# Performance work log

Hardware: AMD Instinct MI355X
Metric: run time of the kernel (lower is better)

## Reference

```python
import jax, jax.numpy as jnp
import numpy as np

B, T, D, HD, O = 32, 2000, 80, 512, 512
H = HD // 2  # per-direction hidden


def setup_inputs() -> dict:
    key = jax.random.key(0)
    ks = jax.random.split(key, 20)
    x = jax.random.normal(ks[0], (B, T, D), jnp.float32)
    x_len = jax.random.randint(ks[1], (B,), T // 2, T + 1)
    s = 1.0 / np.sqrt(H)
    def u(k, shape):
        return jax.random.uniform(k, shape, jnp.float32, -s, s)
    return {
        'x': x, 'x_len': x_len,
        # BLSTM1 (input D), fwd/bwd directions; b is (b_ih + b_hh) combined
        'Wih1f': u(ks[2], (4 * H, D)), 'Whh1f': u(ks[3], (4 * H, H)), 'b1f': u(ks[4], (4 * H,)),
        'Wih1b': u(ks[5], (4 * H, D)), 'Whh1b': u(ks[6], (4 * H, H)), 'b1b': u(ks[7], (4 * H,)),
        # BLSTM2 (input HD)
        'Wih2f': u(ks[8], (4 * H, HD)), 'Whh2f': u(ks[9], (4 * H, H)), 'b2f': u(ks[10], (4 * H,)),
        'Wih2b': u(ks[11], (4 * H, HD)), 'Whh2b': u(ks[12], (4 * H, H)), 'b2b': u(ks[13], (4 * H,)),
        'Wlin': u(ks[14], (O, HD)), 'blin': u(ks[15], (O,)),
    }


def _lstm(x, mask, Wih, Whh, b):
    # x: [B,T,D], mask: [B,T] bool. Packed semantics: state frozen and output 0 at padded steps.
    Bs = x.shape[0]
    Hs = Whh.shape[1]
    xg = jnp.einsum('btd,gd->btg', x, Wih) + b  # precompute input projection [B,T,4H]
    def step(carry, inp):
        h, c = carry
        xt, mt = inp
        g = xt + h @ Whh.T
        i, f, gg, o = jnp.split(g, 4, axis=-1)  # PyTorch gate order i,f,g,o
        c_n = jax.nn.sigmoid(f) * c + jax.nn.sigmoid(i) * jnp.tanh(gg)
        h_n = jax.nn.sigmoid(o) * jnp.tanh(c_n)
        m = mt[:, None]
        h = jnp.where(m, h_n, h)
        c = jnp.where(m, c_n, c)
        return (h, c), h * m
    h0 = jnp.zeros((Bs, Hs), x.dtype)
    _, ys = jax.lax.scan(step, (h0, h0), (xg.transpose(1, 0, 2), mask.T))
    return ys.transpose(1, 0, 2)


def _rev(x, lengths):
    # per-sequence time reversal of the valid prefix
    Ts = x.shape[1]
    t = jnp.arange(Ts)
    idx = jnp.clip(lengths[:, None] - 1 - t[None, :], 0, Ts - 1)
    return jnp.take_along_axis(x, idx[..., None], axis=1)


def _blstm(x, lengths, Wf, Uf, bf, Wb, Ub, bb):
    Ts = x.shape[1]
    mask = jnp.arange(Ts)[None, :] < lengths[:, None]
    fwd = _lstm(x, mask, Wf, Uf, bf)
    bwd = _rev(_lstm(_rev(x, lengths), mask, Wb, Ub, bb), lengths) * mask[..., None]
    return jnp.concatenate([fwd, bwd], axis=-1)


def _pool(x, s):
    # MaxPool1d(kernel=s, stride=s, pad=0) over time of [B,T,C]
    if s == 1:
        return x
    Bs, Ts, Cs = x.shape
    To = Ts // s
    return x[:, :To * s].reshape(Bs, To, s, Cs).max(axis=2)


def reference(x, x_len, Wih1f, Whh1f, b1f, Wih1b, Whh1b, b1b,
              Wih2f, Whh2f, b2f, Wih2b, Whh2b, b2b, Wlin, blin):
    s1, s2 = 2, 1  # closest_factors(time_reduction=2)
    out = _blstm(x, x_len, Wih1f, Whh1f, b1f, Wih1b, Whh1b, b1b)
    out = _pool(out, s1)
    lens = x_len // s1  # (L - k)//s + 1 == L//s when k==s, pad=0, dil=1
    out = _blstm(out, lens, Wih2f, Whh2f, b2f, Wih2b, Whh2b, b2b)
    out = _pool(out, s2)
    lens = lens // s2
    out = out @ Wlin.T + blin  # dropout is identity in eval mode
    return out, lens
```

## Files before the change

### kernel.cpp

```cpp
#include <hip/hip_runtime.h>


typedef _Float16 h2_t __attribute__((ext_vector_type(2)));

constexpr int RC = 10;
constexpr int AC = 15;
constexpr int LC = 7;

__device__ __forceinline__ float dot2acc(unsigned int w, unsigned int h, float acc) {
  h2_t wv = __builtin_bit_cast(h2_t, w);
  h2_t hv = __builtin_bit_cast(h2_t, h);
#if __has_builtin(__builtin_amdgcn_fdot2)
  return __builtin_amdgcn_fdot2(wv, hv, acc, false);
#else
  return acc + (float)wv[0] * (float)hv[0] + (float)wv[1] * (float)hv[1];
#endif
}

__device__ __forceinline__ float dot8(uint4 w, uint4 h, float acc) {
  acc = dot2acc(w.x, h.x, acc);
  acc = dot2acc(w.y, h.y, acc);
  acc = dot2acc(w.z, h.z, acc);
  acc = dot2acc(w.w, h.w, acc);
  return acc;
}

__device__ __forceinline__ float sigf(float x) { return 1.f / (1.f + __expf(-x)); }

__global__ __launch_bounds__(256) void pack_w(const float* __restrict__ W,
                                              uint4* __restrict__ Wp, int K) {
  const int idx = blockIdx.x * 256 + threadIdx.x;
  const int total = (K >> 3) << 10;
  if (idx >= total) return;
  const int g = idx & 1023;
  const int k8 = idx >> 10;
  const float* src = W + (size_t)g * K + k8 * 8;
  h2_t p0, p1, p2, p3;
  p0[0] = (_Float16)src[0]; p0[1] = (_Float16)src[1];
  p1[0] = (_Float16)src[2]; p1[1] = (_Float16)src[3];
  p2[0] = (_Float16)src[4]; p2[1] = (_Float16)src[5];
  p3[0] = (_Float16)src[6]; p3[1] = (_Float16)src[7];
  uint4 o;
  o.x = __builtin_bit_cast(unsigned int, p0);
  o.y = __builtin_bit_cast(unsigned int, p1);
  o.z = __builtin_bit_cast(unsigned int, p2);
  o.w = __builtin_bit_cast(unsigned int, p3);
  Wp[(size_t)k8 * 1024 + g] = o;
}

__global__ __launch_bounds__(256) void pack_flat(const float* __restrict__ src,
                                                 _Float16* __restrict__ dst, int n) {
  const int i = blockIdx.x * 256 + threadIdx.x;
  if (i < n) dst[i] = (_Float16)src[i];
}

__global__ __launch_bounds__(256) void zero16(uint4* __restrict__ p, int n16) {
  const int i = blockIdx.x * 256 + threadIdx.x;
  if (i < n16) { uint4 z; z.x = z.y = z.z = z.w = 0u; p[i] = z; }
}

template <typename AT, typename CT>
__global__ __launch_bounds__(256) void gemm_any(
    const AT* __restrict__ A, const float* __restrict__ B,
    const float* __restrict__ bias, CT* __restrict__ C,
    int M, int N, int K, int Twin, int Tfull, int t0, int REV,
    const int* __restrict__ x_len, int lensh) {
  __shared__ float As[16][128];
  __shared__ float Bs[16][64];
  const int tid = threadIdx.x;
  const int m0 = blockIdx.y * 128, n0 = blockIdx.x * 64;
  const int ra = tid >> 1;
  const int ca = (tid & 1) * 8;
  const int rb = tid >> 2;
  const int cb = (tid & 3) * 4;
  const int ty = tid >> 4;
  const int tx = tid & 15;
  const int am = m0 + ra;
  int arow = am;
  if (Twin > 0) {
    const int bb = am / Twin;
    int ti = t0 + (am - bb * Twin);
    if (REV) {
      const int L = x_len[bb] >> lensh;
      ti = L - 1 - ti;
      ti = ti < 0 ? 0 : ti;
    }
    arow = bb * Tfull + ti;
  }
  float acc[8][4] = {};
  for (int k0 = 0; k0 < K; k0 += 16) {
    float a8[8];
    if constexpr (sizeof(AT) == 2) {
      const uint4 av = *reinterpret_cast<const uint4*>(&A[(size_t)arow * K + k0 + ca]);
      h2_t p0 = __builtin_bit_cast(h2_t, av.x);
      h2_t p1 = __builtin_bit_cast(h2_t, av.y);
      h2_t p2 = __builtin_bit_cast(h2_t, av.z);
      h2_t p3 = __builtin_bit_cast(h2_t, av.w);
      a8[0] = (float)p0[0]; a8[1] = (float)p0[1];
      a8[2] = (float)p1[0]; a8[3] = (float)p1[1];
      a8[4] = (float)p2[0]; a8[5] = (float)p2[1];
      a8[6] = (float)p3[0]; a8[7] = (float)p3[1];
    } else {
      const float4 a0 = *reinterpret_cast<const float4*>(&A[(size_t)arow * K + k0 + ca]);
      const float4 a1 = *reinterpret_cast<const float4*>(&A[(size_t)arow * K + k0 + ca + 4]);
      a8[0] = a0.x; a8[1] = a0.y; a8[2] = a0.z; a8[3] = a0.w;
      a8[4] = a1.x; a8[5] = a1.y; a8[6] = a1.z; a8[7] = a1.w;
    }
    const float4 b0 = *reinterpret_cast<const float4*>(&B[(size_t)(n0 + rb) * K + k0 + cb]);
    __syncthreads();
#pragma unroll
    for (int q = 0; q < 8; ++q) As[ca + q][ra] = a8[q];
    Bs[cb + 0][rb] = b0.x; Bs[cb + 1][rb] = b0.y;
    Bs[cb + 2][rb] = b0.z; Bs[cb + 3][rb] = b0.w;
    __syncthreads();
#pragma unroll
    for (int kk = 0; kk < 16; ++kk) {
      const float4 av0 = *reinterpret_cast<const float4*>(&As[kk][ty * 8]);
      const float4 av1 = *reinterpret_cast<const float4*>(&As[kk][ty * 8 + 4]);
      const float4 bv  = *reinterpret_cast<const float4*>(&Bs[kk][tx * 4]);
      const float a[8] = {av0.x, av0.y, av0.z, av0.w, av1.x, av1.y, av1.z, av1.w};
      const float bb4[4] = {bv.x, bv.y, bv.z, bv.w};
#pragma unroll
      for (int i = 0; i < 8; ++i)
#pragma unroll
        for (int j = 0; j < 4; ++j) acc[i][j] += a[i] * bb4[j];
    }
  }
  const float4 bias4 = *reinterpret_cast<const float4*>(&bias[n0 + tx * 4]);
  const float bb4[4] = {bias4.x, bias4.y, bias4.z, bias4.w};
#pragma unroll
  for (int i = 0; i < 8; ++i) {
    const size_t cidx = (size_t)(m0 + ty * 8 + i) * N + n0 + tx * 4;
    if constexpr (sizeof(CT) == 2) {
      h2_t lo, hi;
      lo[0] = (_Float16)(acc[i][0] + bb4[0]); lo[1] = (_Float16)(acc[i][1] + bb4[1]);
      hi[0] = (_Float16)(acc[i][2] + bb4[2]); hi[1] = (_Float16)(acc[i][3] + bb4[3]);
      uint2 st;
      st.x = __builtin_bit_cast(unsigned int, lo);
      st.y = __builtin_bit_cast(unsigned int, hi);
      *reinterpret_cast<uint2*>(&C[cidx]) = st;
    } else {
      float4 o;
      o.x = acc[i][0] + bb4[0]; o.y = acc[i][1] + bb4[1];
      o.z = acc[i][2] + bb4[2]; o.w = acc[i][3] + bb4[3];
      *reinterpret_cast<float4*>(&C[cidx]) = o;
    }
  }
}

#define AWR(i, src) asm volatile("v_accvgpr_write_b32 %0, %1" : "=a"(agw[i]) : "v"(src))
#define ARD(dst, i) asm volatile("v_accvgpr_read_b32 %0, %1" : "=v"(dst) : "a"(agw[i]))

template <int POOL>
__global__ __launch_bounds__(256, 1) void lstm_oc(
    const _Float16* __restrict__ xgF, const _Float16* __restrict__ xgB,
    const uint4* __restrict__ whhF, const uint4* __restrict__ whhB,
    _Float16* __restrict__ outp, const int* __restrict__ x_len,
    float* __restrict__ stC, _Float16* __restrict__ stH, float* __restrict__ stP,
    int lenshift, int T, int Twin, int s0) {
  const int b = blockIdx.x;
  const int dir = blockIdx.y;
  const int u = threadIdx.x;
  const int len = x_len[b] >> lenshift;
  if (s0 >= len) return;
  const int ns = min(Twin, len - s0);
  const int col0 = dir ? 256 : 0;
  const int Tp = T >> 1;
  const int sidx = (b * 2 + dir) * 256 + u;
  const uint4* whh0 = (dir ? whhB : whhF) + u;
  const _Float16* xg = dir ? xgB : xgF;

  uint4 wreg[RC][4];
#pragma unroll
  for (int k = 0; k < RC; ++k)
#pragma unroll
    for (int g = 0; g < 4; ++g) wreg[k][g] = whh0[(k << 10) + (g << 8)];

  unsigned agw[AC * 16];
#pragma unroll
  for (int k = 0; k < AC; ++k) {
#pragma unroll
    for (int g = 0; g < 4; ++g) {
      const uint4 w = whh0[((RC + k) << 10) + (g << 8)];
      const int base = (k * 4 + g) * 4;
      AWR(base + 0, w.x);
      AWR(base + 1, w.y);
      AWR(base + 2, w.z);
      AWR(base + 3, w.w);
    }
  }

  __shared__ uint4 wlds[LC][4][256];
  __shared__ __align__(16) _Float16 hb[2][256];
#pragma unroll
  for (int lc = 0; lc < LC; ++lc)
#pragma unroll
    for (int g = 0; g < 4; ++g) wlds[lc][g][u] = whh0[((RC + AC + lc) << 10) + (g << 8)];

  hb[0][u] = stH[sidx];
  float c = stC[sidx];
  float hpend = stP[sidx];
  __syncthreads();

  int par = 0;
  for (int j = 0; j < ns; ++j) {
    const int s = s0 + j;
    const int t = dir ? (len - 1 - s) : s;
    const _Float16* xp = xg + ((size_t)b * Twin + j) * 1024 + u;
    const float xi = (float)xp[0];
    const float xf = (float)xp[256];
    const float xgg = (float)xp[512];
    const float xo = (float)xp[768];
    float ai = 0.f, af = 0.f, ag = 0.f, ao = 0.f;
    const uint4* hp = reinterpret_cast<const uint4*>(hb[par]);
#pragma unroll
    for (int k = 0; k < RC; ++k) {
      const uint4 hv = hp[k];
      ai = dot8(wreg[k][0], hv, ai);
      af = dot8(wreg[k][1], hv, af);
      ag = dot8(wreg[k][2], hv, ag);
      ao = dot8(wreg[k][3], hv, ao);
    }
#pragma unroll
    for (int k = 0; k < AC; ++k) {
      const uint4 hv = hp[RC + k];
#pragma unroll
      for (int g = 0; g < 4; ++g) {
        uint4 w;
        const int base = (k * 4 + g) * 4;
        ARD(w.x, base + 0);
        ARD(w.y, base + 1);
        ARD(w.z, base + 2);
        ARD(w.w, base + 3);
        if (g == 0) ai = dot8(w, hv, ai);
        else if (g == 1) af = dot8(w, hv, af);
        else if (g == 2) ag = dot8(w, hv, ag);
        else ao = dot8(w, hv, ao);
      }
    }
#pragma unroll
    for (int lc = 0; lc < LC; ++lc) {
      const uint4 hv = hp[RC + AC + lc];
      ai = dot8(wlds[lc][0][u], hv, ai);
      af = dot8(wlds[lc][1][u], hv, af);
      ag = dot8(wlds[lc][2][u], hv, ag);
      ao = dot8(wlds[lc][3][u], hv, ao);
    }
    ai += xi; af += xf; ag += xgg; ao += xo;
    const float gi = sigf(ai);
    const float gf = sigf(af);
    const float gc = 2.f * sigf(2.f * ag) - 1.f;
    const float go = sigf(ao);
    c = gf * c + gi * gc;
    const float h = go * (2.f * sigf(2.f * c) - 1.f);
    if (POOL) {
      if (dir == 0) {
        if (t & 1) outp[((size_t)b * Tp + (t >> 1)) * 512 + col0 + u] = (_Float16)fmaxf(hpend, h);
        else hpend = h;
      } else {
        if (t & 1) hpend = h;
        else outp[((size_t)b * Tp + (t >> 1)) * 512 + col0 + u] = (_Float16)fmaxf(h, hpend);
      }
    } else {
      outp[((size_t)b * T + t) * 512 + col0 + u] = (_Float16)h;
    }
    hb[par ^ 1][u] = (_Float16)h;
    par ^= 1;
    __syncthreads();
  }
  stH[sidx] = hb[par][u];
  stC[sidx] = c;
  stP[sidx] = hpend;
  if (POOL && dir == 0 && (len & 1) && (len - s0) <= Twin) {
    outp[((size_t)b * Tp + ((len - 1) >> 1)) * 512 + col0 + u] = (_Float16)fmaxf(hpend, 0.f);
  }
}

template <int POOL>
__global__ __launch_bounds__(256) void lstm_stream(
    const uint4* __restrict__ xh, int kx8,
    const uint4* __restrict__ wih_f, const uint4* __restrict__ wih_b,
    const float* __restrict__ bias_f, const float* __restrict__ bias_b,
    const uint4* __restrict__ whh_f, const uint4* __restrict__ whh_b,
    _Float16* __restrict__ outp, const int* __restrict__ x_len,
    int lenshift, int T) {
  const int b = blockIdx.x;
  const int dir = blockIdx.y;
  const int u = threadIdx.x;
  const int len = x_len[b] >> lenshift;
  const uint4* wih = dir ? wih_b : wih_f;
  const float* bias = dir ? bias_b : bias_f;
  const uint4* whh0 = (dir ? whh_b : whh_f) + u;
  const int col0 = dir ? 256 : 0;
  const float bi = bias[u], bff = bias[u + 256], bg = bias[u + 512], bo = bias[u + 768];
  __shared__ __align__(16) _Float16 hbuf[2][256];
  hbuf[0][u] = (_Float16)0.f;
  float c = 0.f, hpend = 0.f;
  __syncthreads();
  int cur = 0;
  const int Tp = T >> 1;
  for (int s = 0; s < len; ++s) {
    const int t = dir ? (len - 1 - s) : s;
    float ai = bi, af = bff, ag = bg, ao = bo;
    const uint4* xr = xh + ((size_t)b * T + t) * kx8;
    const uint4* wir = wih + u;
    for (int k8 = 0; k8 < kx8; ++k8) {
      const uint4 xv = xr[k8];
      ai = dot8(wir[0],   xv, ai);
      af = dot8(wir[256], xv, af);
      ag = dot8(wir[512], xv, ag);
      ao = dot8(wir[768], xv, ao);
      wir += 1024;
    }
    const uint4* hp = reinterpret_cast<const uint4*>(hbuf[cur]);
#pragma unroll 4
    for (int k8 = 0; k8 < 32; ++k8) {
      const uint4 hv = hp[k8];
      const uint4* wr = whh0 + (k8 << 10);
      ai = dot8(wr[0],   hv, ai);
      af = dot8(wr[256], hv, af);
      ag = dot8(wr[512], hv, ag);
      ao = dot8(wr[768], hv, ao);
    }
    const float gi = sigf(ai);
    const float gf = sigf(af);
    const float gg = 2.f * sigf(2.f * ag) - 1.f;
    const float go = sigf(ao);
    c = gf * c + gi * gg;
    const float h = go * (2.f * sigf(2.f * c) - 1.f);
    if (POOL) {
      if (dir == 0) {
        if (t & 1) outp[((size_t)b * Tp + (t >> 1)) * 512 + col0 + u] = (_Float16)fmaxf(hpend, h);
        else hpend = h;
      } else {
        if (t & 1) hpend = h;
        else outp[((size_t)b * Tp + (t >> 1)) * 512 + col0 + u] = (_Float16)fmaxf(h, hpend);
      }
    } else {
      outp[((size_t)b * T + t) * 512 + col0 + u] = (_Float16)h;
    }
    hbuf[cur ^ 1][u] = (_Float16)h;
    cur ^= 1;
    __syncthreads();
  }
  if (POOL && dir == 0 && (len & 1)) {
    outp[((size_t)b * Tp + ((len - 1) >> 1)) * 512 + col0 + u] = (_Float16)fmaxf(hpend, 0.f);
  }
}

__global__ void lens_k(const int* __restrict__ x_len, float* __restrict__ dst) {
  const int b = threadIdx.x;
  if (b < 32) dst[b] = (float)(x_len[b] >> 1);
}

extern "C" void kernel_launch(void* const* d_in, const int* in_sizes, int n_in,
                              void* d_out, int out_size, void* d_ws, size_t ws_size,
                              hipStream_t stream) {
  (void)in_sizes; (void)n_in; (void)out_size;
  const float* x     = (const float*)d_in[0];
  const int*   x_len = (const int*)d_in[1];
  const float* Wih1f = (const float*)d_in[2];
  const float* Whh1f = (const float*)d_in[3];
  const float* b1f   = (const float*)d_in[4];
  const float* Wih1b = (const float*)d_in[5];
  const float* Whh1b = (const float*)d_in[6];
  const float* b1b   = (const float*)d_in[7];
  const float* Wih2f = (const float*)d_in[8];
  const float* Whh2f = (const float*)d_in[9];
  const float* b2f   = (const float*)d_in[10];
  const float* Wih2b = (const float*)d_in[11];
  const float* Whh2b = (const float*)d_in[12];
  const float* b2b   = (const float*)d_in[13];
  const float* Wlin  = (const float*)d_in[14];
  const float* blin  = (const float*)d_in[15];
  float* outF = (float*)d_out;

  char* w = (char*)d_ws;
  size_t off = 0;
  auto alloc = [&](size_t bytes) -> void* {
    void* p = w + off;
    off += (bytes + 255) & ~(size_t)255;
    return p;
  };
  uint4* wp_hh1f = (uint4*)alloc(524288);
  uint4* wp_hh1b = (uint4*)alloc(524288);
  uint4* wp_hh2f = (uint4*)alloc(524288);
  uint4* wp_hh2b = (uint4*)alloc(524288);
  uint4* wp_ih1f = (uint4*)alloc(163840);
  uint4* wp_ih1b = (uint4*)alloc(163840);
  uint4* wp_ih2f = (uint4*)alloc(1048576);
  uint4* wp_ih2b = (uint4*)alloc(1048576);
  _Float16* pooled = (_Float16*)alloc(32768000);
  _Float16* out2   = (_Float16*)alloc(32768000);
  float*    stC1 = (float*)alloc(65536);
  _Float16* stH1 = (_Float16*)alloc(32768);
  float*    stP1 = (float*)alloc(65536);
  float*    stC2 = (float*)alloc(65536);
  _Float16* stH2 = (_Float16*)alloc(32768);
  float*    stP2 = (float*)alloc(65536);
  const size_t var_off = off;
  _Float16* varr = (_Float16*)(w + var_off);
  _Float16* xgwF = varr;
  _Float16* xgwB = varr + 16384000;
  _Float16* xg2f = varr;
  _Float16* xg2b = varr + 32768000;
  _Float16* x_h  = varr;

  const int main_tier = (ws_size >= var_off + 131072000ULL) ? 1 : 0;

  pack_w<<<128, 256, 0, stream>>>(Whh1f, wp_hh1f, 256);
  pack_w<<<128, 256, 0, stream>>>(Whh1b, wp_hh1b, 256);
  pack_w<<<128, 256, 0, stream>>>(Whh2f, wp_hh2f, 256);
  pack_w<<<128, 256, 0, stream>>>(Whh2b, wp_hh2b, 256);
  zero16<<<16000, 256, 0, stream>>>((uint4*)pooled, 4096000);
  zero16<<<80, 256, 0, stream>>>((uint4*)stC1, 20480);

  if (main_tier) {
    for (int w4 = 0; w4 < 4; ++w4) {
      const int t0 = 500 * w4;
      gemm_any<float, _Float16><<<dim3(16, 125), 256, 0, stream>>>(
          x, Wih1f, b1f, xgwF, 16000, 1024, 80, 500, 2000, t0, 0, x_len, 0);
      gemm_any<float, _Float16><<<dim3(16, 125), 256, 0, stream>>>(
          x, Wih1b, b1b, xgwB, 16000, 1024, 80, 500, 2000, t0, 1, x_len, 0);
      lstm_oc<1><<<dim3(32, 2), 256, 0, stream>>>(
          xgwF, xgwB, wp_hh1f, wp_hh1b, pooled, x_len,
          stC1, stH1, stP1, 0, 2000, 500, t0);
    }
    gemm_any<_Float16, _Float16><<<dim3(16, 250), 256, 0, stream>>>(
        pooled, Wih2f, b2f, xg2f, 32000, 1024, 512, 0, 0, 0, 0, nullptr, 0);
    gemm_any<_Float16, _Float16><<<dim3(16, 250), 256, 0, stream>>>(
        pooled, Wih2b, b2b, xg2b, 32000, 1024, 512, 0, 0, 0, 0, nullptr, 0);
    lstm_oc<0><<<dim3(32, 2), 256, 0, stream>>>(
        xg2f, xg2b, wp_hh2f, wp_hh2b, out2, x_len,
        stC2, stH2, stP2, 1, 1000, 1000, 0);
  } else {
    pack_w<<<40, 256, 0, stream>>>(Wih1f, wp_ih1f, 80);
    pack_w<<<40, 256, 0, stream>>>(Wih1b, wp_ih1b, 80);
    pack_w<<<256, 256, 0, stream>>>(Wih2f, wp_ih2f, 512);
    pack_w<<<256, 256, 0, stream>>>(Wih2b, wp_ih2b, 512);
    pack_flat<<<20000, 256, 0, stream>>>(x, x_h, 5120000);
    lstm_stream<1><<<dim3(32, 2), 256, 0, stream>>>(
        (const uint4*)x_h, 10, wp_ih1f, wp_ih1b, b1f, b1b,
        wp_hh1f, wp_hh1b, pooled, x_len, 0, 2000);
    lstm_stream<0><<<dim3(32, 2), 256, 0, stream>>>(
        (const uint4*)pooled, 64, wp_ih2f, wp_ih2b, b2f, b2b,
        wp_hh2f, wp_hh2b, out2, x_len, 1, 1000);
  }

  gemm_any<_Float16, float><<<dim3(8, 250), 256, 0, stream>>>(
      out2, Wlin, blin, outF, 32000, 512, 512, 0, 0, 0, 0, nullptr, 0);
  lens_k<<<1, 32, 0, stream>>>(x_len, outF + (size_t)16384000);
}
```

Before: 9.008 ms.

## Split LSTM recurrence across 512 threads with two gate rows each

```diff
diff --git a/kernel.cpp b/kernel.cpp
--- a/kernel.cpp
+++ b/kernel.cpp
@@ -3,9 +3,8 @@
 
 typedef _Float16 h2_t __attribute__((ext_vector_type(2)));
 
-constexpr int RC = 10;
-constexpr int AC = 15;
-constexpr int LC = 7;
+constexpr int VC = 24;
+constexpr int LCH = 32 - VC;
 
 __device__ __forceinline__ float dot2acc(unsigned int w, unsigned int h, float acc) {
   h2_t wv = __builtin_bit_cast(h2_t, w);
@@ -25,7 +24,7 @@
   return acc;
 }
 
-__device__ __forceinline__ float sigf(float x) { return 1.f / (1.f + __expf(-x)); }
+__device__ __forceinline__ float sigf(float x) { return 1.f / (1.f + expf(-x)); }
 
 __global__ __launch_bounds__(256) void pack_w(const float* __restrict__ W,
                                               uint4* __restrict__ Wp, int K) {
@@ -148,131 +147,106 @@
   }
 }
 
-#define AWR(i, src) asm volatile("v_accvgpr_write_b32 %0, %1" : "=a"(agw[i]) : "v"(src))
-#define ARD(dst, i) asm volatile("v_accvgpr_read_b32 %0, %1" : "=v"(dst) : "a"(agw[i]))
-
 template <int POOL>
-__global__ __launch_bounds__(256, 1) void lstm_oc(
-    const _Float16* __restrict__ xgF, const _Float16* __restrict__ xgB,
+__global__ __launch_bounds__(512, 2) void lstm2(
+    const float* __restrict__ xgF, const float* __restrict__ xgB,
     const uint4* __restrict__ whhF, const uint4* __restrict__ whhB,
     _Float16* __restrict__ outp, const int* __restrict__ x_len,
     float* __restrict__ stC, _Float16* __restrict__ stH, float* __restrict__ stP,
     int lenshift, int T, int Twin, int s0) {
   const int b = blockIdx.x;
   const int dir = blockIdx.y;
-  const int u = threadIdx.x;
+  const int t_ = threadIdx.x;
+  const int u = t_ & 255;
+  const int p = t_ >> 8;
   const int len = x_len[b] >> lenshift;
   if (s0 >= len) return;
   const int ns = min(Twin, len - s0);
   const int col0 = dir ? 256 : 0;
   const int Tp = T >> 1;
   const int sidx = (b * 2 + dir) * 256 + u;
-  const uint4* whh0 = (dir ? whhB : whhF) + u;
-  const _Float16* xg = dir ? xgB : xgF;
-
-  uint4 wreg[RC][4];
-#pragma unroll
-  for (int k = 0; k < RC; ++k)
-#pragma unroll
-    for (int g = 0; g < 4; ++g) wreg[k][g] = whh0[(k << 10) + (g << 8)];
-
-  unsigned agw[AC * 16];
-#pragma unroll
-  for (int k = 0; k < AC; ++k) {
-#pragma unroll
-    for (int g = 0; g < 4; ++g) {
-      const uint4 w = whh0[((RC + k) << 10) + (g << 8)];
-      const int base = (k * 4 + g) * 4;
-      AWR(base + 0, w.x);
-      AWR(base + 1, w.y);
-      AWR(base + 2, w.z);
-      AWR(base + 3, w.w);
-    }
-  }
-
-  __shared__ uint4 wlds[LC][4][256];
+  const uint4* whh = dir ? whhB : whhF;
+  const float* xg = dir ? xgB : xgF;
+  const int r0 = p * 512 + u;
+  const int r1 = p * 512 + 256 + u;
+
+  uint4 w0[VC], w1[VC];
+#pragma unroll
+  for (int k = 0; k < VC; ++k) {
+    w0[k] = whh[(k << 10) + r0];
+    w1[k] = whh[(k << 10) + r1];
+  }
+  __shared__ uint4 wlds[LCH][1024];
   __shared__ __align__(16) _Float16 hb[2][256];
-#pragma unroll
-  for (int lc = 0; lc < LC; ++lc)
-#pragma unroll
-    for (int g = 0; g < 4; ++g) wlds[lc][g][u] = whh0[((RC + AC + lc) << 10) + (g << 8)];
-
-  hb[0][u] = stH[sidx];
-  float c = stC[sidx];
-  float hpend = stP[sidx];
+  __shared__ float2 gl[256];
+#pragma unroll
+  for (int kc = 0; kc < LCH; ++kc) {
+    wlds[kc][r0] = whh[((VC + kc) << 10) + r0];
+    wlds[kc][r1] = whh[((VC + kc) << 10) + r1];
+  }
+  if (t_ < 256) hb[0][t_] = stH[(b * 2 + dir) * 256 + t_];
+  float c = 0.f, hpend = 0.f;
+  if (p == 0) { c = stC[sidx]; hpend = stP[sidx]; }
   __syncthreads();
 
   int par = 0;
+  const float* xq = xg + (size_t)b * Twin * 1024 + p * 512 + u;
+  float xa = xq[0];
+  float xb2 = xq[256];
   for (int j = 0; j < ns; ++j) {
     const int s = s0 + j;
     const int t = dir ? (len - 1 - s) : s;
-    const _Float16* xp = xg + ((size_t)b * Twin + j) * 1024 + u;
-    const float xi = (float)xp[0];
-    const float xf = (float)xp[256];
-    const float xgg = (float)xp[512];
-    const float xo = (float)xp[768];
-    float ai = 0.f, af = 0.f, ag = 0.f, ao = 0.f;
+    float a0 = xa, a1 = xb2;
     const uint4* hp = reinterpret_cast<const uint4*>(hb[par]);
 #pragma unroll
-    for (int k = 0; k < RC; ++k) {
+    for (int k = 0; k < VC; ++k) {
       const uint4 hv = hp[k];
-      ai = dot8(wreg[k][0], hv, ai);
-      af = dot8(wreg[k][1], hv, af);
-      ag = dot8(wreg[k][2], hv, ag);
-      ao = dot8(wreg[k][3], hv, ao);
-    }
-#pragma unroll
-    for (int k = 0; k < AC; ++k) {
-      const uint4 hv = hp[RC + k];
-#pragma unroll
-      for (int g = 0; g < 4; ++g) {
-        uint4 w;
-        const int base = (k * 4 + g) * 4;
-        ARD(w.x, base + 0);
-        ARD(w.y, base + 1);
-        ARD(w.z, base + 2);
-        ARD(w.w, base + 3);
-        if (g == 0) ai = dot8(w, hv, ai);
-        else if (g == 1) af = dot8(w, hv, af);
-        else if (g == 2) ag = dot8(w, hv, ag);
-        else ao = dot8(w, hv, ao);
+      a0 = dot8(w0[k], hv, a0);
+      a1 = dot8(w1[k], hv, a1);
+    }
+#pragma unroll
+    for (int kc = 0; kc < LCH; ++kc) {
+      const uint4 hv = hp[VC + kc];
+      a0 = dot8(wlds[kc][r0], hv, a0);
+      a1 = dot8(wlds[kc][r1], hv, a1);
+    }
+    if (j + 1 < ns) {
+      xa = xq[(size_t)(j + 1) * 1024];
+      xb2 = xq[(size_t)(j + 1) * 1024 + 256];
+    }
+    if (p) { gl[u].x = a0; gl[u].y = a1; }
+    __syncthreads();
+    if (!p) {
+      const float2 g2 = gl[u];
+      const float gi = sigf(a0);
+      const float gf = sigf(a1);
+      const float gc = tanhf(g2.x);
+      const float go = sigf(g2.y);
+      c = gf * c + gi * gc;
+      const float h = go * tanhf(c);
+      hb[par ^ 1][u] = (_Float16)h;
+      if (POOL) {
+        if (dir == 0) {
+          if (t & 1) outp[((size_t)b * Tp + (t >> 1)) * 512 + col0 + u] = (_Float16)fmaxf(hpend, h);
+          else hpend = h;
+        } else {
+          if (t & 1) hpend = h;
+          else outp[((size_t)b * Tp + (t >> 1)) * 512 + col0 + u] = (_Float16)fmaxf(h, hpend);
+        }
+      } else {
+        outp[((size_t)b * T + t) * 512 + col0 + u] = (_Float16)h;
       }
     }
-#pragma unroll
-    for (int lc = 0; lc < LC; ++lc) {
-      const uint4 hv = hp[RC + AC + lc];
-      ai = dot8(wlds[lc][0][u], hv, ai);
-      af = dot8(wlds[lc][1][u], hv, af);
-      ag = dot8(wlds[lc][2][u], hv, ag);
-      ao = dot8(wlds[lc][3][u], hv, ao);
-    }
-    ai += xi; af += xf; ag += xgg; ao += xo;
-    const float gi = sigf(ai);
-    const float gf = sigf(af);
-    const float gc = 2.f * sigf(2.f * ag) - 1.f;
-    const float go = sigf(ao);
-    c = gf * c + gi * gc;
-    const float h = go * (2.f * sigf(2.f * c) - 1.f);
-    if (POOL) {
-      if (dir == 0) {
-        if (t & 1) outp[((size_t)b * Tp + (t >> 1)) * 512 + col0 + u] = (_Float16)fmaxf(hpend, h);
-        else hpend = h;
-      } else {
-        if (t & 1) hpend = h;
-        else outp[((size_t)b * Tp + (t >> 1)) * 512 + col0 + u] = (_Float16)fmaxf(h, hpend);
-      }
-    } else {
-      outp[((size_t)b * T + t) * 512 + col0 + u] = (_Float16)h;
-    }
-    hb[par ^ 1][u] = (_Float16)h;
+    __syncthreads();
     par ^= 1;
-    __syncthreads();
-  }
-  stH[sidx] = hb[par][u];
-  stC[sidx] = c;
-  stP[sidx] = hpend;
-  if (POOL && dir == 0 && (len & 1) && (len - s0) <= Twin) {
-    outp[((size_t)b * Tp + ((len - 1) >> 1)) * 512 + col0 + u] = (_Float16)fmaxf(hpend, 0.f);
+  }
+  if (p == 0) {
+    stH[sidx] = hb[par][u];
+    stC[sidx] = c;
+    stP[sidx] = hpend;
+    if (POOL && dir == 0 && (len & 1) && (len - s0) <= Twin) {
+      outp[((size_t)b * Tp + ((len - 1) >> 1)) * 512 + col0 + u] = (_Float16)fmaxf(hpend, 0.f);
+    }
   }
 }
 
@@ -324,10 +298,10 @@
     }
     const float gi = sigf(ai);
     const float gf = sigf(af);
-    const float gg = 2.f * sigf(2.f * ag) - 1.f;
+    const float gg = tanhf(ag);
     const float go = sigf(ao);
     c = gf * c + gi * gg;
-    const float h = go * (2.f * sigf(2.f * c) - 1.f);
+    const float h = go * tanhf(c);
     if (POOL) {
       if (dir == 0) {
         if (t & 1) outp[((size_t)b * Tp + (t >> 1)) * 512 + col0 + u] = (_Float16)fmaxf(hpend, h);
@@ -399,12 +373,10 @@
   _Float16* stH2 = (_Float16*)alloc(32768);
   float*    stP2 = (float*)alloc(65536);
   const size_t var_off = off;
-  _Float16* varr = (_Float16*)(w + var_off);
-  _Float16* xgwF = varr;
-  _Float16* xgwB = varr + 16384000;
-  _Float16* xg2f = varr;
-  _Float16* xg2b = varr + 32768000;
-  _Float16* x_h  = varr;
+  float* varrF = (float*)(w + var_off);
+  float* xgwF = varrF;
+  float* xgwB = varrF + 16384000;
+  _Float16* x_h = (_Float16*)(w + var_off);
 
   const int main_tier = (ws_size >= var_off + 131072000ULL) ? 1 : 0;
 
@@ -418,21 +390,24 @@
   if (main_tier) {
     for (int w4 = 0; w4 < 4; ++w4) {
       const int t0 = 500 * w4;
-      gemm_any<float, _Float16><<<dim3(16, 125), 256, 0, stream>>>(
+      gemm_any<float, float><<<dim3(16, 125), 256, 0, stream>>>(
           x, Wih1f, b1f, xgwF, 16000, 1024, 80, 500, 2000, t0, 0, x_len, 0);
-      gemm_any<float, _Float16><<<dim3(16, 125), 256, 0, stream>>>(
+      gemm_any<float, float><<<dim3(16, 125), 256, 0, stream>>>(
           x, Wih1b, b1b, xgwB, 16000, 1024, 80, 500, 2000, t0, 1, x_len, 0);
-      lstm_oc<1><<<dim3(32, 2), 256, 0, stream>>>(
+      lstm2<1><<<dim3(32, 2), 512, 0, stream>>>(
           xgwF, xgwB, wp_hh1f, wp_hh1b, pooled, x_len,
           stC1, stH1, stP1, 0, 2000, 500, t0);
     }
-    gemm_any<_Float16, _Float16><<<dim3(16, 250), 256, 0, stream>>>(
-        pooled, Wih2f, b2f, xg2f, 32000, 1024, 512, 0, 0, 0, 0, nullptr, 0);
-    gemm_any<_Float16, _Float16><<<dim3(16, 250), 256, 0, stream>>>(
-        pooled, Wih2b, b2b, xg2b, 32000, 1024, 512, 0, 0, 0, 0, nullptr, 0);
-    lstm_oc<0><<<dim3(32, 2), 256, 0, stream>>>(
-        xg2f, xg2b, wp_hh2f, wp_hh2b, out2, x_len,
-        stC2, stH2, stP2, 1, 1000, 1000, 0);
+    for (int w2 = 0; w2 < 2; ++w2) {
+      const int t0 = 500 * w2;
+      gemm_any<_Float16, float><<<dim3(16, 125), 256, 0, stream>>>(
+          pooled, Wih2f, b2f, xgwF, 16000, 1024, 512, 500, 1000, t0, 0, x_len, 1);
+      gemm_any<_Float16, float><<<dim3(16, 125), 256, 0, stream>>>(
+          pooled, Wih2b, b2b, xgwB, 16000, 1024, 512, 500, 1000, t0, 1, x_len, 1);
+      lstm2<0><<<dim3(32, 2), 512, 0, stream>>>(
+          xgwF, xgwB, wp_hh2f, wp_hh2b, out2, x_len,
+          stC2, stH2, stP2, 1, 1000, 500, t0);
+    }
   } else {
     pack_w<<<40, 256, 0, stream>>>(Wih1f, wp_ih1f, 80);
     pack_w<<<40, 256, 0, stream>>>(Wih1b, wp_ih1b, 80);
```

After: 30.69 ms. 3.41x slower.
